# Kernel optimization log

Measured on AMD Instinct MI355X. Metric: run time of the kernel, lower is better.

The kernel has to match this reference:

```python
import jax, jax.numpy as jnp
import numpy as np

NUM_HEADS = 16
HEAD_DIM = 64
EMB = 1024


def setup_inputs() -> dict:
    key = jax.random.key(0)
    k1, k2, k3 = jax.random.split(key, 3)
    x = jax.random.normal(k1, (4, 1024, EMB), dtype=jnp.float32)
    W_qkv = jax.random.normal(k2, (EMB, 3 * NUM_HEADS * HEAD_DIM), dtype=jnp.float32) * (EMB ** -0.5)
    b_qkv = jnp.zeros((3 * NUM_HEADS * HEAD_DIM,), dtype=jnp.float32)
    W_out = jax.random.normal(k3, (NUM_HEADS * HEAD_DIM, EMB), dtype=jnp.float32) * ((NUM_HEADS * HEAD_DIM) ** -0.5)
    b_out = jnp.zeros((EMB,), dtype=jnp.float32)
    return {"x": x, "W_qkv": W_qkv, "b_qkv": b_qkv, "W_out": W_out, "b_out": b_out}


def reference(x, W_qkv, b_qkv, W_out, b_out):
    B, N, D = x.shape
    qkv = x @ W_qkv + b_qkv                      # B N 3*H*hd
    # torch.split order in the source is K, Q, V
    K, Q, V = jnp.split(qkv, 3, axis=-1)
    def heads(t):  # B N (H hd) -> B H N hd
        return t.reshape(B, N, NUM_HEADS, HEAD_DIM).transpose(0, 2, 1, 3)
    K, Q, V = heads(K), heads(Q), heads(V)
    scores = jnp.einsum('bhqd,bhkd->bhqk', Q, K) / (HEAD_DIM ** 0.5)
    att = jax.nn.softmax(scores, axis=-1)        # dropout p=0.0 -> identity
    out = jnp.einsum('bhqk,bhkd->bhqd', att, V)  # B H N hd
    out = out.transpose(0, 2, 1, 3).reshape(B, N, NUM_HEADS * HEAD_DIM)
    return out @ W_out + b_out
```

## Files before the change

### kernel.cpp

```cpp
#include <hip/hip_runtime.h>
#include <hip/hip_bf16.h>
#include <cstddef>
#include <cmath>


typedef _Float16 f16x4 __attribute__((ext_vector_type(4)));
typedef _Float16 f16x8 __attribute__((ext_vector_type(8)));
typedef float    f32x4 __attribute__((ext_vector_type(4)));

#define LOG2E 1.4426950408889634f

__device__ __forceinline__ void gload_lds16(const void* g, void* l) {
    __builtin_amdgcn_global_load_lds(
        (const __attribute__((address_space(1))) unsigned int*)g,
        (__attribute__((address_space(3))) unsigned int*)l, 16, 0, 0);
}

__global__ __launch_bounds__(256) void cvt_f32_f16(
    const float* __restrict__ in, _Float16* __restrict__ out, int n8)
{
    int i = blockIdx.x * 256 + threadIdx.x;
    if (i < n8) {
        const float4* p = (const float4*)in;
        float4 v0 = p[i * 2], v1 = p[i * 2 + 1];
        f16x8 o;
        o[0] = (_Float16)v0.x; o[1] = (_Float16)v0.y; o[2] = (_Float16)v0.z; o[3] = (_Float16)v0.w;
        o[4] = (_Float16)v1.x; o[5] = (_Float16)v1.y; o[6] = (_Float16)v1.z; o[7] = (_Float16)v1.w;
        *(f16x8*)(out + (size_t)i * 8) = o;
    }
}

__global__ __launch_bounds__(256) void transpose_f32_to_f16(
    const float* __restrict__ in, _Float16* __restrict__ out, int R, int C)
{
    __shared__ float tile[64][65];
    int r0 = blockIdx.y * 64, c0 = blockIdx.x * 64;
    int t = threadIdx.x;
#pragma unroll
    for (int p = 0; p < 4; ++p) {
        int lin = p * 256 + t;
        int row = lin >> 4;
        int c4 = (lin & 15) * 4;
        float4 v = *(const float4*)(in + (size_t)(r0 + row) * C + c0 + c4);
        tile[row][c4] = v.x; tile[row][c4 + 1] = v.y;
        tile[row][c4 + 2] = v.z; tile[row][c4 + 3] = v.w;
    }
    __syncthreads();
#pragma unroll
    for (int p = 0; p < 2; ++p) {
        int lin = p * 256 + t;
        int oc = lin >> 3;
        int ch = (lin & 7) * 8;
        f16x8 o;
#pragma unroll
        for (int e = 0; e < 8; ++e) o[e] = (_Float16)tile[ch + e][oc];
        *(f16x8*)(out + (size_t)(c0 + oc) * R + r0 + ch) = o;
    }
}

__global__ __launch_bounds__(256) void transpose_f16(
    const _Float16* __restrict__ in, _Float16* __restrict__ out, int R, int C)
{
    __shared__ _Float16 tile[64][72];
    const _Float16* inh = in + (size_t)blockIdx.z * R * C;
    _Float16* outh = out + (size_t)blockIdx.z * R * C;
    int r0 = blockIdx.y * 64, c0 = blockIdx.x * 64;
    int t = threadIdx.x;
#pragma unroll
    for (int p = 0; p < 2; ++p) {
        int lin = p * 256 + t;
        int row = lin >> 3;
        int ch = (lin & 7) * 8;
        f16x8 v = *(const f16x8*)(inh + (size_t)(r0 + row) * C + c0 + ch);
        *(f16x8*)&tile[row][ch] = v;
    }
    __syncthreads();
#pragma unroll
    for (int p = 0; p < 2; ++p) {
        int lin = p * 256 + t;
        int oc = lin >> 3;
        int ch = (lin & 7) * 8;
        f16x8 o;
#pragma unroll
        for (int e = 0; e < 8; ++e) o[e] = tile[ch + e][oc];
        *(f16x8*)(outh + (size_t)(c0 + oc) * R + r0 + ch) = o;
    }
}

template <int EPI>
__global__ __launch_bounds__(256) void gemm_f16(
    const _Float16* __restrict__ A, const _Float16* __restrict__ Bt,
    const float* __restrict__ bias, float* __restrict__ Cout,
    _Float16* __restrict__ Kh, _Float16* __restrict__ Qh, _Float16* __restrict__ Vh,
    int M, int Nn, int Kk)
{
    __shared__ _Float16 As[128 * 64];
    __shared__ _Float16 Bs[128 * 64];
    int m0 = blockIdx.y * 128, n0 = blockIdx.x * 128;
    int t = threadIdx.x, lane = t & 63, wid = t >> 6;
    int wr = (wid >> 1) * 64, wc = (wid & 1) * 64;
    int lr = lane & 15, lg = lane >> 4;

    f32x4 acc[4][4] = {};

    for (int k0 = 0; k0 < Kk; k0 += 64) {
#pragma unroll
        for (int p = 0; p < 4; ++p) {
            int c = p * 256 + t;
            int row = c >> 3, col = (c & 7) * 8;
            int ubase = (p * 256 + wid * 64) * 8;
            gload_lds16(A  + (size_t)(m0 + row) * Kk + k0 + col, &As[ubase]);
            gload_lds16(Bt + (size_t)(n0 + row) * Kk + k0 + col, &Bs[ubase]);
        }
        __syncthreads();
#pragma unroll
        for (int kk = 0; kk < 2; ++kk) {
            f16x8 af[4], bfr[4];
#pragma unroll
            for (int i = 0; i < 4; ++i) {
                af[i]  = *(const f16x8*)&As[(wr + i * 16 + lr) * 64 + kk * 32 + lg * 8];
                bfr[i] = *(const f16x8*)&Bs[(wc + i * 16 + lr) * 64 + kk * 32 + lg * 8];
            }
#pragma unroll
            for (int i = 0; i < 4; ++i)
#pragma unroll
                for (int jn = 0; jn < 4; ++jn)
                    acc[i][jn] = __builtin_amdgcn_mfma_f32_16x16x32_f16(
                        af[i], bfr[jn], acc[i][jn], 0, 0, 0);
        }
        __syncthreads();
    }

#pragma unroll
    for (int i = 0; i < 4; ++i)
#pragma unroll
        for (int jn = 0; jn < 4; ++jn) {
            int gc = n0 + wc + jn * 16 + lr;
            float bv = bias[gc];
#pragma unroll
            for (int j = 0; j < 4; ++j) {
                int gr = m0 + wr + i * 16 + lg * 4 + j;
                float v = acc[i][jn][j] + bv;
                if constexpr (EPI == 0) {
                    Cout[(size_t)gr * Nn + gc] = v;
                } else {
                    int sec = gc >> 10, idx = gc & 1023;
                    int h = idx >> 6, d = idx & 63;
                    int bb = gr >> 10, pos = gr & 1023;
                    size_t hoff = (((size_t)(bb * 16 + h) * 1024) + pos) * 64 + d;
                    if (sec == 0)      Kh[hoff] = (_Float16)v;
                    else if (sec == 1) Qh[hoff] = (_Float16)(v * (0.125f * LOG2E));
                    else               Vh[hoff] = (_Float16)v;
                }
            }
        }
}

__global__ __launch_bounds__(256) void attn_kernel(
    const _Float16* __restrict__ Qh, const _Float16* __restrict__ Kh,
    const _Float16* __restrict__ Vt, _Float16* __restrict__ attO)
{
    __shared__ _Float16 Ks[2][64 * 64];
    __shared__ _Float16 Vs[2][64 * 64];
    __shared__ _Float16 Pl[4][16 * 64];

    int wg = blockIdx.x;
    int swz = (wg & 7) * 128 + (wg >> 3);
    int bh = swz >> 4, qt = swz & 15;
    int b = bh >> 4, h = bh & 15;

    int tid = threadIdx.x;
    int wid = tid >> 6, lane = tid & 63;
    int lr = lane & 15, lg = lane >> 4;
    int q0 = qt * 64 + wid * 16;
    const _Float16* Qb = Qh + (size_t)bh * (1024 * 64);
    const _Float16* Kb = Kh + (size_t)bh * (1024 * 64);
    const _Float16* Vb = Vt + (size_t)bh * (64 * 1024);

    int c0 = tid, c1 = 256 + tid;
    int r0 = c0 >> 3, sc0 = ((c0 & 7) * 16) ^ ((r0 & 7) << 4);
    int r1 = c1 >> 3, sc1 = ((c1 & 7) * 16) ^ ((r1 & 7) << 4);
    int ub0 = (wid * 64) * 8, ub1 = (256 + wid * 64) * 8;

    f16x8 qf0 = *(const f16x8*)(Qb + (size_t)(q0 + lr) * 64 + lg * 8);
    f16x8 qf1 = *(const f16x8*)(Qb + (size_t)(q0 + lr) * 64 + 32 + lg * 8);

    float m = -1e30f, l = 0.f;
    f32x4 o[4] = {};
    int xr = (lr & 7) << 4;

    gload_lds16(Kb + (size_t)r0 * 64 + (sc0 >> 1), &Ks[0][ub0]);
    gload_lds16(Kb + (size_t)r1 * 64 + (sc1 >> 1), &Ks[0][ub1]);
    gload_lds16(Vb + (size_t)r0 * 1024 + (sc0 >> 1), &Vs[0][ub0]);
    gload_lds16(Vb + (size_t)r1 * 1024 + (sc1 >> 1), &Vs[0][ub1]);
    __syncthreads();

    for (int t = 0; t < 16; ++t) {
        int cur = t & 1;
        if (t < 15) {
            int kn = (t + 1) * 64;
            gload_lds16(Kb + (size_t)(kn + r0) * 64 + (sc0 >> 1), &Ks[cur ^ 1][ub0]);
            gload_lds16(Kb + (size_t)(kn + r1) * 64 + (sc1 >> 1), &Ks[cur ^ 1][ub1]);
            gload_lds16(Vb + (size_t)r0 * 1024 + kn + (sc0 >> 1), &Vs[cur ^ 1][ub0]);
            gload_lds16(Vb + (size_t)r1 * 1024 + kn + (sc1 >> 1), &Vs[cur ^ 1][ub1]);
        }
        const _Float16* Kc = &Ks[cur][0];
        const _Float16* Vc = &Vs[cur][0];

        f32x4 s[4] = {};
#pragma unroll
        for (int kb = 0; kb < 4; ++kb) {
            const char* krow = (const char*)(Kc + (kb * 16 + lr) * 64);
            f16x8 kf0 = *(const f16x8*)(krow + ((lg * 16) ^ xr));
            f16x8 kf1 = *(const f16x8*)(krow + ((64 + lg * 16) ^ xr));
            s[kb] = __builtin_amdgcn_mfma_f32_16x16x32_f16(kf0, qf0, s[kb], 0, 0, 0);
            s[kb] = __builtin_amdgcn_mfma_f32_16x16x32_f16(kf1, qf1, s[kb], 0, 0, 0);
        }
        float a0 = fmaxf(fmaxf(s[0][0], s[0][1]), fmaxf(s[0][2], s[0][3]));
        float a1 = fmaxf(fmaxf(s[1][0], s[1][1]), fmaxf(s[1][2], s[1][3]));
        float a2 = fmaxf(fmaxf(s[2][0], s[2][1]), fmaxf(s[2][2], s[2][3]));
        float a3 = fmaxf(fmaxf(s[3][0], s[3][1]), fmaxf(s[3][2], s[3][3]));
        float pmax = fmaxf(fmaxf(a0, a1), fmaxf(a2, a3));
        pmax = fmaxf(pmax, __shfl_xor(pmax, 16));
        pmax = fmaxf(pmax, __shfl_xor(pmax, 32));
        float mnew = fmaxf(m, pmax);
        float corr = exp2f(m - mnew);
#pragma unroll
        for (int kb = 0; kb < 4; ++kb)
#pragma unroll
            for (int j = 0; j < 4; ++j)
                s[kb][j] = exp2f(s[kb][j] - mnew);
        float rr0 = (s[0][0] + s[0][1]) + (s[0][2] + s[0][3]);
        float rr1 = (s[1][0] + s[1][1]) + (s[1][2] + s[1][3]);
        float rr2 = (s[2][0] + s[2][1]) + (s[2][2] + s[2][3]);
        float rr3 = (s[3][0] + s[3][1]) + (s[3][2] + s[3][3]);
        float rs = (rr0 + rr1) + (rr2 + rr3);
        rs += __shfl_xor(rs, 16);
        rs += __shfl_xor(rs, 32);
        l = l * corr + rs;
        m = mnew;
#pragma unroll
        for (int db = 0; db < 4; ++db)
#pragma unroll
            for (int j = 0; j < 4; ++j) o[db][j] *= corr;

        char* prow = (char*)&Pl[wid][lr * 64];
#pragma unroll
        for (int kb = 0; kb < 4; ++kb) {
            f16x4 w;
#pragma unroll
            for (int j = 0; j < 4; ++j) w[j] = (_Float16)s[kb][j];
            *(f16x4*)(prow + ((kb * 32 + lg * 8) ^ xr)) = w;
        }
        f16x8 pf0 = *(const f16x8*)(prow + ((lg * 16) ^ xr));
        f16x8 pf1 = *(const f16x8*)(prow + ((64 + lg * 16) ^ xr));

#pragma unroll
        for (int db = 0; db < 4; ++db) {
            const char* vrow = (const char*)(Vc + (db * 16 + lr) * 64);
            f16x8 vf0 = *(const f16x8*)(vrow + ((lg * 16) ^ xr));
            f16x8 vf1 = *(const f16x8*)(vrow + ((64 + lg * 16) ^ xr));
            o[db] = __builtin_amdgcn_mfma_f32_16x16x32_f16(vf0, pf0, o[db], 0, 0, 0);
            o[db] = __builtin_amdgcn_mfma_f32_16x16x32_f16(vf1, pf1, o[db], 0, 0, 0);
        }
        __syncthreads();
    }

    float li = 1.f / l;
#pragma unroll
    for (int db = 0; db < 4; ++db) {
        f16x4 w;
#pragma unroll
        for (int j = 0; j < 4; ++j) w[j] = (_Float16)(o[db][j] * li);
        *(f16x4*)(attO + ((size_t)b * 1024 + q0 + lr) * 1024 + h * 64 + db * 16 + lg * 4) = w;
    }
}

extern "C" void kernel_launch(void* const* d_in, const int* in_sizes, int n_in,
                              void* d_out, int out_size, void* d_ws, size_t ws_size,
                              hipStream_t stream)
{
    const float* x    = (const float*)d_in[0];
    const float* Wqkv = (const float*)d_in[1];
    const float* bqkv = (const float*)d_in[2];
    const float* Wout = (const float*)d_in[3];
    const float* bout = (const float*)d_in[4];
    float* out = (float*)d_out;

    char* ws = (char*)d_ws;
    _Float16* xb    = (_Float16*)(ws);
    _Float16* Vt    = (_Float16*)(ws);
    _Float16* Wqkvt = (_Float16*)(ws + ((size_t)8  << 20));
    _Float16* Woutt = (_Float16*)(ws + ((size_t)14 << 20));
    _Float16* Qh    = (_Float16*)(ws + ((size_t)16 << 20));
    _Float16* Kh    = (_Float16*)(ws + ((size_t)24 << 20));
    _Float16* Vh    = (_Float16*)(ws + ((size_t)32 << 20));
    _Float16* attO  = (_Float16*)(ws + ((size_t)40 << 20));

    cvt_f32_f16<<<2048, 256, 0, stream>>>(x, xb, 4096 * 1024 / 8);
    transpose_f32_to_f16<<<dim3(48, 16), 256, 0, stream>>>(Wqkv, Wqkvt, 1024, 3072);
    transpose_f32_to_f16<<<dim3(16, 16), 256, 0, stream>>>(Wout, Woutt, 1024, 1024);

    gemm_f16<1><<<dim3(24, 32), 256, 0, stream>>>(
        xb, Wqkvt, bqkv, nullptr, Kh, Qh, Vh, 4096, 3072, 1024);

    transpose_f16<<<dim3(1, 16, 64), 256, 0, stream>>>(Vh, Vt, 1024, 64);

    attn_kernel<<<1024, 256, 0, stream>>>(Qh, Kh, Vt, attO);

    gemm_f16<0><<<dim3(8, 32), 256, 0, stream>>>(
        attO, Woutt, bout, out, nullptr, nullptr, nullptr, 4096, 1024, 1024);
}
```

Before: 210.4 us.

## Double-buffer LDS tiles in GEMM and remap workgroups across XCDs

Shared-memory tiles in the f16 GEMM kernel are now double-buffered, so the next K tile is prefetched with global_load_lds while MFMAs run on the current one. This is meant to hide global load latency behind compute. Workgroup IDs are also remapped in groups of 8 so neighbouring tiles land on the same XCD, aiming for better L2 reuse. LDS use doubles to 64KB per block, which may lower occupancy, and the remap assumes the workgroup count is divisible by 8.

Result: no change. 211.3 us (+0.4%).

```diff
diff --git a/kernel.cpp b/kernel.cpp
--- a/kernel.cpp
+++ b/kernel.cpp
@@ -94,32 +94,54 @@
     _Float16* __restrict__ Kh, _Float16* __restrict__ Qh, _Float16* __restrict__ Vh,
     int M, int Nn, int Kk)
 {
-    __shared__ _Float16 As[128 * 64];
-    __shared__ _Float16 Bs[128 * 64];
-    int m0 = blockIdx.y * 128, n0 = blockIdx.x * 128;
+    __shared__ _Float16 As[2][128 * 64];
+    __shared__ _Float16 Bs[2][128 * 64];
+
+    int lin = blockIdx.y * gridDim.x + blockIdx.x;
+    int nwg = gridDim.x * gridDim.y;
+    int lin2 = (lin & 7) * (nwg >> 3) + (lin >> 3);
+    int bx = lin2 % gridDim.x, by = lin2 / gridDim.x;
+    int m0 = by * 128, n0 = bx * 128;
+
     int t = threadIdx.x, lane = t & 63, wid = t >> 6;
     int wr = (wid >> 1) * 64, wc = (wid & 1) * 64;
     int lr = lane & 15, lg = lane >> 4;
 
     f32x4 acc[4][4] = {};
-
-    for (int k0 = 0; k0 < Kk; k0 += 64) {
-#pragma unroll
-        for (int p = 0; p < 4; ++p) {
-            int c = p * 256 + t;
-            int row = c >> 3, col = (c & 7) * 8;
-            int ubase = (p * 256 + wid * 64) * 8;
-            gload_lds16(A  + (size_t)(m0 + row) * Kk + k0 + col, &As[ubase]);
-            gload_lds16(Bt + (size_t)(n0 + row) * Kk + k0 + col, &Bs[ubase]);
-        }
-        __syncthreads();
+    int nt = Kk >> 6;
+
+#pragma unroll
+    for (int p = 0; p < 4; ++p) {
+        int c = p * 256 + t;
+        int row = c >> 3, col = (c & 7) * 8;
+        int ubase = (p * 256 + wid * 64) * 8;
+        gload_lds16(A  + (size_t)(m0 + row) * Kk + col, &As[0][ubase]);
+        gload_lds16(Bt + (size_t)(n0 + row) * Kk + col, &Bs[0][ubase]);
+    }
+    __syncthreads();
+
+    for (int tt = 0; tt < nt; ++tt) {
+        int cur = tt & 1;
+        if (tt + 1 < nt) {
+            int k0 = (tt + 1) * 64;
+#pragma unroll
+            for (int p = 0; p < 4; ++p) {
+                int c = p * 256 + t;
+                int row = c >> 3, col = (c & 7) * 8;
+                int ubase = (p * 256 + wid * 64) * 8;
+                gload_lds16(A  + (size_t)(m0 + row) * Kk + k0 + col, &As[cur ^ 1][ubase]);
+                gload_lds16(Bt + (size_t)(n0 + row) * Kk + k0 + col, &Bs[cur ^ 1][ubase]);
+            }
+        }
+        const _Float16* Ac = &As[cur][0];
+        const _Float16* Bc = &Bs[cur][0];
 #pragma unroll
         for (int kk = 0; kk < 2; ++kk) {
             f16x8 af[4], bfr[4];
 #pragma unroll
             for (int i = 0; i < 4; ++i) {
-                af[i]  = *(const f16x8*)&As[(wr + i * 16 + lr) * 64 + kk * 32 + lg * 8];
-                bfr[i] = *(const f16x8*)&Bs[(wc + i * 16 + lr) * 64 + kk * 32 + lg * 8];
+                af[i]  = *(const f16x8*)&Ac[(wr + i * 16 + lr) * 64 + kk * 32 + lg * 8];
+                bfr[i] = *(const f16x8*)&Bc[(wc + i * 16 + lr) * 64 + kk * 32 + lg * 8];
             }
 #pragma unroll
             for (int i = 0; i < 4; ++i)
```
